# Performance work log

Measured on AMD Instinct MI355X. Metric: run time of the kernel, lower is better.

Reference implementation:

```python
import jax, jax.numpy as jnp
import numpy as np

B, N, DIM = 2, 2048, 2048
H, KVH, HD = 16, 4, 128
N_REP = H // KVH
SCALE = np.float32(HD ** -0.5)


def setup_inputs() -> dict:
    key = jax.random.key(0)
    ks = jax.random.split(key, 5)
    x = jax.random.normal(ks[0], (B, N, DIM), dtype=jnp.float32)
    mask = jnp.tril(jnp.ones((N, N), dtype=jnp.int32))[None, None]  # [1,1,N,N] causal
    Wq = jax.random.normal(ks[1], (DIM, H * HD), dtype=jnp.float32) * (DIM ** -0.5)
    Wk = jax.random.normal(ks[2], (DIM, KVH * HD), dtype=jnp.float32) * (DIM ** -0.5)
    Wv = jax.random.normal(ks[3], (DIM, KVH * HD), dtype=jnp.float32) * (DIM ** -0.5)
    Wo = jax.random.normal(ks[4], (H * HD, DIM), dtype=jnp.float32) * ((H * HD) ** -0.5)
    return {"x": x, "mask": mask, "Wq": Wq, "Wk": Wk, "Wv": Wv, "Wo": Wo}


def reference(x, mask, Wq, Wk, Wv, Wo):
    Bx, Nx, _ = x.shape
    # projections -> [B, heads, N, head_dim]
    q = (x @ Wq).reshape(Bx, Nx, H, HD).transpose(0, 2, 1, 3)
    k = (x @ Wk).reshape(Bx, Nx, KVH, HD).transpose(0, 2, 1, 3)
    v = (x @ Wv).reshape(Bx, Nx, KVH, HD).transpose(0, 2, 1, 3)
    # repeat_interleave KV heads to match query heads (GQA)
    k = jnp.repeat(k, N_REP, axis=1)
    v = jnp.repeat(v, N_REP, axis=1)
    attn = jnp.einsum('bhqd,bhkd->bhqk', q, k) * SCALE
    attn = jnp.where(mask == 0, jnp.float32(-jnp.inf), attn)
    attn = jax.nn.softmax(attn, axis=-1)
    out = jnp.einsum('bhqk,bhkd->bhqd', attn, v)
    out = out.transpose(0, 2, 1, 3).reshape(Bx, Nx, H * HD)
    return out @ Wo
```

## Files before the change

### kernel.cpp

```cpp
#include <hip/hip_runtime.h>
#include <hip/hip_bf16.h>
#include <math.h>

typedef __bf16 bf16;
typedef bf16 bf16x8 __attribute__((ext_vector_type(8)));
typedef bf16 bf16x4v __attribute__((ext_vector_type(4)));
typedef float f32x4 __attribute__((ext_vector_type(4)));

#define GLD16(g, l) __builtin_amdgcn_global_load_lds(                          \
    (__attribute__((address_space(1))) void*)(g),                              \
    (__attribute__((address_space(3))) void*)(l), 16, 0, 0)

#define MFMA16(a, b, c) __builtin_amdgcn_mfma_f32_16x16x32_bf16((a), (b), (c), 0, 0, 0)

__device__ __forceinline__ f32x4 shfl_xor4(f32x4 a, int m) {
  f32x4 r;
  #pragma unroll
  for (int i = 0; i < 4; i++) r[i] = __shfl_xor(a[i], m);
  return r;
}

__global__ void cast_f32_bf16(const float* __restrict__ in, bf16* __restrict__ out, int n4) {
  int i = blockIdx.x * blockDim.x + threadIdx.x;
  if (i < n4) {
    float4 v = ((const float4*)in)[i];
    bf16x4v o;
    o.x = (bf16)v.x; o.y = (bf16)v.y; o.z = (bf16)v.z; o.w = (bf16)v.w;
    ((bf16x4v*)out)[i] = o;
  }
}

__global__ void transpose_cast(const float* __restrict__ in, bf16* __restrict__ out,
                               int colsIn, int outStride, int outRowOff) {
  __shared__ float t[32][33];
  int c0 = blockIdx.x * 32, r0 = blockIdx.y * 32;
  int tx = threadIdx.x, ty = threadIdx.y;
  #pragma unroll
  for (int i = 0; i < 32; i += 8)
    t[ty + i][tx] = in[(size_t)(r0 + ty + i) * colsIn + (c0 + tx)];
  __syncthreads();
  #pragma unroll
  for (int i = 0; i < 32; i += 8)
    out[(size_t)(outRowOff + c0 + ty + i) * outStride + (r0 + tx)] = (bf16)t[tx][ty + i];
}

template <typename OutT>
__global__ __launch_bounds__(256, 2) void gemm_bt(const bf16* __restrict__ A,
                                                  const bf16* __restrict__ Bt,
                                                  OutT* __restrict__ C,
                                                  int M, int N, int K) {
  __shared__ __attribute__((aligned(16))) bf16 As[128 * 32];
  __shared__ __attribute__((aligned(16))) bf16 Bs[128 * 32];
  const int tid = threadIdx.x;
  const int lane = tid & 63;
  const int wave = tid >> 6;
  const int wm = wave >> 1, wn = wave & 1;
  const int l15 = lane & 15, quad = lane >> 4;
  const int rowBase = blockIdx.y * 128;
  const int colBase = blockIdx.x * 128;

  f32x4 acc[4][4] = {};

  const int cb0 = wave * 64;
  const int c0 = cb0 + lane;
  const int c1 = c0 + 256;
  const bf16* a0 = A + (size_t)(rowBase + (c0 >> 2)) * K + (c0 & 3) * 8;
  const bf16* a1 = A + (size_t)(rowBase + (c1 >> 2)) * K + (c1 & 3) * 8;
  const bf16* b0 = Bt + (size_t)(colBase + (c0 >> 2)) * K + (c0 & 3) * 8;
  const bf16* b1 = Bt + (size_t)(colBase + (c1 >> 2)) * K + (c1 & 3) * 8;
  bf16* lA0 = &As[cb0 * 8];
  bf16* lA1 = &As[(cb0 + 256) * 8];
  bf16* lB0 = &Bs[cb0 * 8];
  bf16* lB1 = &Bs[(cb0 + 256) * 8];

  for (int k0 = 0; k0 < K; k0 += 32) {
    GLD16(a0 + k0, lA0);
    GLD16(a1 + k0, lA1);
    GLD16(b0 + k0, lB0);
    GLD16(b1 + k0, lB1);
    __syncthreads();
    bf16x8 af[4], bfr[4];
    #pragma unroll
    for (int i = 0; i < 4; i++)
      af[i] = *(const bf16x8*)&As[(wm * 64 + i * 16 + l15) * 32 + quad * 8];
    #pragma unroll
    for (int i = 0; i < 4; i++)
      bfr[i] = *(const bf16x8*)&Bs[(wn * 64 + i * 16 + l15) * 32 + quad * 8];
    #pragma unroll
    for (int i = 0; i < 4; i++)
      #pragma unroll
      for (int j = 0; j < 4; j++)
        acc[i][j] = MFMA16(af[i], bfr[j], acc[i][j]);
    __syncthreads();
  }

  #pragma unroll
  for (int i = 0; i < 4; i++) {
    int row = rowBase + wm * 64 + i * 16 + quad * 4;
    #pragma unroll
    for (int j = 0; j < 4; j++) {
      int col = colBase + wn * 64 + j * 16 + l15;
      #pragma unroll
      for (int r = 0; r < 4; r++)
        C[(size_t)(row + r) * N + col] = (OutT)acc[i][j][r];
    }
  }
}

#define SCALE_F 0.08838834764831845f
#define L2E 1.4426950408889634f
#define MASKV (-1e30f)

__global__ __launch_bounds__(256, 2) void gqa_attn(const bf16* __restrict__ QKV,
                                                   bf16* __restrict__ Obf) {
  __shared__ __attribute__((aligned(16))) bf16 Kl[64 * 152];
  __shared__ __attribute__((aligned(16))) bf16 Vt[128 * 72];
  __shared__ __attribute__((aligned(16))) bf16 Pl[4][32 * 72];

  const int tid = threadIdx.x;
  const int lane = tid & 63;
  const int wave = tid >> 6;
  const int l15 = lane & 15, quad = lane >> 4;

  int bi = blockIdx.x;
  int bh = bi & 31;
  int jj = (bi & 255) >> 5;
  int qt = (bi < 256) ? (8 + jj) : (7 - jj);
  int b = bh >> 4, h = bh & 15, kvh = h >> 2;
  int q0 = qt * 128;

  const size_t rs = 3072;
  const bf16* Qb = QKV + (size_t)b * 2048 * rs + h * 128;
  const bf16* Kb = QKV + (size_t)b * 2048 * rs + 2048 + kvh * 128;
  const bf16* Vb = QKV + (size_t)b * 2048 * rs + 2560 + kvh * 128;

  bf16x8 qf[2][4];
  #pragma unroll
  for (int mt = 0; mt < 2; mt++) {
    int row = q0 + wave * 32 + mt * 16 + l15;
    #pragma unroll
    for (int ks = 0; ks < 4; ks++)
      qf[mt][ks] = *(const bf16x8*)&Qb[(size_t)row * rs + ks * 32 + quad * 8];
  }

  f32x4 oacc[2][8] = {};
  f32x4 mrow[2], lrow[2];
  #pragma unroll
  for (int mt = 0; mt < 2; mt++)
    #pragma unroll
    for (int r = 0; r < 4; r++) { mrow[mt][r] = MASKV; lrow[mt][r] = 0.f; }

  const int nkt = 2 * qt + 2;
  for (int kt = 0; kt < nkt; kt++) {
    const int k0 = kt * 64;
    __syncthreads();
    #pragma unroll
    for (int it = 0; it < 4; it++) {
      int c = it * 256 + tid;
      int key = c >> 4, hc = c & 15;
      bf16x8 v = *(const bf16x8*)&Kb[(size_t)(k0 + key) * rs + hc * 8];
      *(bf16x8*)&Kl[key * 152 + hc * 8] = v;
    }
    #pragma unroll
    for (int it = 0; it < 4; it++) {
      int c = it * 256 + tid;
      int key = c & 63, hc = c >> 6;
      bf16x8 v = *(const bf16x8*)&Vb[(size_t)(k0 + key) * rs + hc * 8];
      #pragma unroll
      for (int j2 = 0; j2 < 8; j2++) Vt[(hc * 8 + j2) * 72 + key] = v[j2];
    }
    __syncthreads();

    if (k0 > q0 + wave * 32 + 31) continue;

    f32x4 s[2][4] = {};
    #pragma unroll
    for (int nt = 0; nt < 4; nt++) {
      #pragma unroll
      for (int ks = 0; ks < 4; ks++) {
        bf16x8 kf = *(const bf16x8*)&Kl[(nt * 16 + l15) * 152 + ks * 32 + quad * 8];
        s[0][nt] = MFMA16(qf[0][ks], kf, s[0][nt]);
        s[1][nt] = MFMA16(qf[1][ks], kf, s[1][nt]);
      }
    }
    bool diag = (kt >= nkt - 2);
    #pragma unroll
    for (int mt = 0; mt < 2; mt++)
      #pragma unroll
      for (int nt = 0; nt < 4; nt++)
        #pragma unroll
        for (int r = 0; r < 4; r++) {
          float v = s[mt][nt][r] * SCALE_F;
          if (diag) {
            int col = k0 + nt * 16 + l15;
            int row = q0 + wave * 32 + mt * 16 + quad * 4 + r;
            if (col > row) v = MASKV;
          }
          s[mt][nt][r] = v;
        }
    #pragma unroll
    for (int mt = 0; mt < 2; mt++) {
      f32x4 mx = s[mt][0];
      #pragma unroll
      for (int nt = 1; nt < 4; nt++)
        #pragma unroll
        for (int r = 0; r < 4; r++) mx[r] = fmaxf(mx[r], s[mt][nt][r]);
      #pragma unroll
      for (int d = 1; d < 16; d <<= 1) {
        f32x4 o = shfl_xor4(mx, d);
        #pragma unroll
        for (int r = 0; r < 4; r++) mx[r] = fmaxf(mx[r], o[r]);
      }
      f32x4 mnew, alpha;
      #pragma unroll
      for (int r = 0; r < 4; r++) {
        mnew[r] = fmaxf(mrow[mt][r], mx[r]);
        alpha[r] = exp2f((mrow[mt][r] - mnew[r]) * L2E);
      }
      f32x4 rsum = {0.f, 0.f, 0.f, 0.f};
      #pragma unroll
      for (int nt = 0; nt < 4; nt++)
        #pragma unroll
        for (int r = 0; r < 4; r++) {
          float p = exp2f((s[mt][nt][r] - mnew[r]) * L2E);
          s[mt][nt][r] = p;
          rsum[r] += p;
        }
      #pragma unroll
      for (int d = 1; d < 16; d <<= 1) rsum += shfl_xor4(rsum, d);
      #pragma unroll
      for (int r = 0; r < 4; r++) {
        lrow[mt][r] = lrow[mt][r] * alpha[r] + rsum[r];
        mrow[mt][r] = mnew[r];
      }
      #pragma unroll
      for (int no = 0; no < 8; no++)
        #pragma unroll
        for (int r = 0; r < 4; r++) oacc[mt][no][r] *= alpha[r];
      #pragma unroll
      for (int nt = 0; nt < 4; nt++)
        #pragma unroll
        for (int r = 0; r < 4; r++)
          Pl[wave][(mt * 16 + quad * 4 + r) * 72 + nt * 16 + l15] = (bf16)s[mt][nt][r];
    }
    #pragma unroll
    for (int ks2 = 0; ks2 < 2; ks2++) {
      bf16x8 pf0 = *(const bf16x8*)&Pl[wave][(l15) * 72 + ks2 * 32 + quad * 8];
      bf16x8 pf1 = *(const bf16x8*)&Pl[wave][(16 + l15) * 72 + ks2 * 32 + quad * 8];
      #pragma unroll
      for (int no = 0; no < 8; no++) {
        bf16x8 vf = *(const bf16x8*)&Vt[(no * 16 + l15) * 72 + ks2 * 32 + quad * 8];
        oacc[0][no] = MFMA16(pf0, vf, oacc[0][no]);
        oacc[1][no] = MFMA16(pf1, vf, oacc[1][no]);
      }
    }
  }

  #pragma unroll
  for (int mt = 0; mt < 2; mt++) {
    f32x4 linv;
    #pragma unroll
    for (int r = 0; r < 4; r++) linv[r] = 1.0f / lrow[mt][r];
    int row = q0 + wave * 32 + mt * 16 + quad * 4;
    #pragma unroll
    for (int no = 0; no < 8; no++) {
      int col = h * 128 + no * 16 + l15;
      #pragma unroll
      for (int r = 0; r < 4; r++)
        Obf[(size_t)(b * 2048 + row + r) * 2048 + col] = (bf16)(oacc[mt][no][r] * linv[r]);
    }
  }
}

extern "C" void kernel_launch(void* const* d_in, const int* in_sizes, int n_in,
                              void* d_out, int out_size, void* d_ws, size_t ws_size,
                              hipStream_t stream) {
  const float* x  = (const float*)d_in[0];
  const float* Wq = (const float*)d_in[2];
  const float* Wk = (const float*)d_in[3];
  const float* Wv = (const float*)d_in[4];
  const float* Wo = (const float*)d_in[5];
  float* out = (float*)d_out;

  bf16* Xb    = (bf16*)d_ws;
  bf16* Wqkvt = Xb + 8388608;
  bf16* Wot   = Wqkvt + 6291456;
  bf16* QKV   = Wot + 4194304;
  bf16* Obf   = QKV + 12582912;

  cast_f32_bf16<<<8192, 256, 0, stream>>>(x, Xb, 2097152);
  dim3 tb(32, 8);
  transpose_cast<<<dim3(64, 64), tb, 0, stream>>>(Wq, Wqkvt, 2048, 2048, 0);
  transpose_cast<<<dim3(16, 64), tb, 0, stream>>>(Wk, Wqkvt, 512, 2048, 2048);
  transpose_cast<<<dim3(16, 64), tb, 0, stream>>>(Wv, Wqkvt, 512, 2048, 2560);
  transpose_cast<<<dim3(64, 64), tb, 0, stream>>>(Wo, Wot, 2048, 2048, 0);

  gemm_bt<bf16><<<dim3(24, 32), 256, 0, stream>>>(Xb, Wqkvt, QKV, 4096, 3072, 2048);
  gqa_attn<<<512, 256, 0, stream>>>(QKV, Obf);
  gemm_bt<float><<<dim3(16, 32), 256, 0, stream>>>(Obf, Wot, out, 4096, 2048, 2048);
}
```

Measured before the change: 368.8 us.

## Pre-transpose V, load K/V tiles via direct-to-LDS loads with XOR swizzle

Adds a separate kernel that transposes V into a head-major [d, n] buffer. The attention kernel can then fill its K and V tiles with asynchronous global_load_lds 16-byte copies into XOR-swizzled LDS, replacing the register round trip and scalar scatter transpose of V. The softmax scale and log2(e) are folded into Wq during the weight cast, and a native exp2 builtin is used, which removes per-element multiplies. The cost is an extra kernel launch plus one read and write of V, and bf16 rounding of the pre-scaled Wq differs slightly from the original.

```diff
diff --git a/kernel.cpp b/kernel.cpp
--- a/kernel.cpp
+++ b/kernel.cpp
@@ -12,6 +12,12 @@
     (__attribute__((address_space(3))) void*)(l), 16, 0, 0)
 
 #define MFMA16(a, b, c) __builtin_amdgcn_mfma_f32_16x16x32_bf16((a), (b), (c), 0, 0, 0)
+
+#if __has_builtin(__builtin_amdgcn_exp2f)
+#define EXP2F(x) __builtin_amdgcn_exp2f(x)
+#else
+#define EXP2F(x) exp2f(x)
+#endif
 
 __device__ __forceinline__ f32x4 shfl_xor4(f32x4 a, int m) {
   f32x4 r;
@@ -31,7 +37,7 @@
 }
 
 __global__ void transpose_cast(const float* __restrict__ in, bf16* __restrict__ out,
-                               int colsIn, int outStride, int outRowOff) {
+                               int colsIn, int outStride, int outRowOff, float scale) {
   __shared__ float t[32][33];
   int c0 = blockIdx.x * 32, r0 = blockIdx.y * 32;
   int tx = threadIdx.x, ty = threadIdx.y;
@@ -41,7 +47,24 @@
   __syncthreads();
   #pragma unroll
   for (int i = 0; i < 32; i += 8)
-    out[(size_t)(outRowOff + c0 + ty + i) * outStride + (r0 + tx)] = (bf16)t[tx][ty + i];
+    out[(size_t)(outRowOff + c0 + ty + i) * outStride + (r0 + tx)] = (bf16)(t[tx][ty + i] * scale);
+}
+
+__global__ void transpose_v(const bf16* __restrict__ QKV, bf16* __restrict__ Vg) {
+  __shared__ bf16 t[32][34];
+  int n0 = blockIdx.x * 32, d0 = blockIdx.y * 32;
+  int bk = blockIdx.z;
+  int b = bk >> 2, kvh = bk & 3;
+  const bf16* src = QKV + (size_t)b * 2048 * 3072 + 2560 + kvh * 128;
+  bf16* dst = Vg + (size_t)bk * 128 * 2048;
+  int tx = threadIdx.x, ty = threadIdx.y;
+  #pragma unroll
+  for (int i = 0; i < 32; i += 8)
+    t[ty + i][tx] = src[(size_t)(n0 + ty + i) * 3072 + (d0 + tx)];
+  __syncthreads();
+  #pragma unroll
+  for (int i = 0; i < 32; i += 8)
+    dst[(size_t)(d0 + ty + i) * 2048 + (n0 + tx)] = t[tx][ty + i];
 }
 
 template <typename OutT>
@@ -107,15 +130,14 @@
   }
 }
 
-#define SCALE_F 0.08838834764831845f
-#define L2E 1.4426950408889634f
 #define MASKV (-1e30f)
 
 __global__ __launch_bounds__(256, 2) void gqa_attn(const bf16* __restrict__ QKV,
+                                                   const bf16* __restrict__ Vg,
                                                    bf16* __restrict__ Obf) {
-  __shared__ __attribute__((aligned(16))) bf16 Kl[64 * 152];
-  __shared__ __attribute__((aligned(16))) bf16 Vt[128 * 72];
-  __shared__ __attribute__((aligned(16))) bf16 Pl[4][32 * 72];
+  __shared__ __attribute__((aligned(16))) bf16 Kl[64 * 128];
+  __shared__ __attribute__((aligned(16))) bf16 Vt[128 * 64];
+  __shared__ __attribute__((aligned(16))) bf16 Pl[4][32 * 68];
 
   const int tid = threadIdx.x;
   const int lane = tid & 63;
@@ -130,9 +152,9 @@
   int q0 = qt * 128;
 
   const size_t rs = 3072;
-  const bf16* Qb = QKV + (size_t)b * 2048 * rs + h * 128;
-  const bf16* Kb = QKV + (size_t)b * 2048 * rs + 2048 + kvh * 128;
-  const bf16* Vb = QKV + (size_t)b * 2048 * rs + 2560 + kvh * 128;
+  const bf16* Qb  = QKV + (size_t)b * 2048 * rs + h * 128;
+  const bf16* Kb  = QKV + (size_t)b * 2048 * rs + 2048 + kvh * 128;
+  const bf16* Vgb = Vg + (size_t)(b * 4 + kvh) * 128 * 2048;
 
   bf16x8 qf[2][4];
   #pragma unroll
@@ -143,6 +165,20 @@
       qf[mt][ks] = *(const bf16x8*)&Qb[(size_t)row * rs + ks * 32 + quad * 8];
   }
 
+  const bf16* kp[4]; const bf16* vp[4];
+  bf16* kl[4]; bf16* vl[4];
+  #pragma unroll
+  for (int t = 0; t < 4; t++) {
+    int keyl = wave * 16 + t * 4 + (lane >> 4);
+    int ck = (lane & 15) ^ (4 * (t & 1) + (lane >> 4));
+    kp[t] = Kb + (size_t)keyl * rs + ck * 8;
+    kl[t] = &Kl[(wave * 16 + t * 4) * 128];
+    int dl = wave * 32 + t * 8 + (lane >> 3);
+    int cv = (lane & 7) ^ (lane >> 3);
+    vp[t] = Vgb + (size_t)dl * 2048 + cv * 8;
+    vl[t] = &Vt[(wave * 32 + t * 8) * 64];
+  }
+
   f32x4 oacc[2][8] = {};
   f32x4 mrow[2], lrow[2];
   #pragma unroll
@@ -151,53 +187,42 @@
     for (int r = 0; r < 4; r++) { mrow[mt][r] = MASKV; lrow[mt][r] = 0.f; }
 
   const int nkt = 2 * qt + 2;
+  const int myrow_hi = q0 + wave * 32 + 31;
   for (int kt = 0; kt < nkt; kt++) {
     const int k0 = kt * 64;
     __syncthreads();
     #pragma unroll
-    for (int it = 0; it < 4; it++) {
-      int c = it * 256 + tid;
-      int key = c >> 4, hc = c & 15;
-      bf16x8 v = *(const bf16x8*)&Kb[(size_t)(k0 + key) * rs + hc * 8];
-      *(bf16x8*)&Kl[key * 152 + hc * 8] = v;
-    }
-    #pragma unroll
-    for (int it = 0; it < 4; it++) {
-      int c = it * 256 + tid;
-      int key = c & 63, hc = c >> 6;
-      bf16x8 v = *(const bf16x8*)&Vb[(size_t)(k0 + key) * rs + hc * 8];
-      #pragma unroll
-      for (int j2 = 0; j2 < 8; j2++) Vt[(hc * 8 + j2) * 72 + key] = v[j2];
-    }
+    for (int t = 0; t < 4; t++) { GLD16(kp[t], kl[t]); kp[t] += 64 * rs; }
+    #pragma unroll
+    for (int t = 0; t < 4; t++) { GLD16(vp[t], vl[t]); vp[t] += 64; }
     __syncthreads();
 
-    if (k0 > q0 + wave * 32 + 31) continue;
+    if (k0 > myrow_hi) continue;
 
     f32x4 s[2][4] = {};
     #pragma unroll
-    for (int nt = 0; nt < 4; nt++) {
-      #pragma unroll
-      for (int ks = 0; ks < 4; ks++) {
-        bf16x8 kf = *(const bf16x8*)&Kl[(nt * 16 + l15) * 152 + ks * 32 + quad * 8];
+    for (int ks = 0; ks < 4; ks++) {
+      #pragma unroll
+      for (int nt = 0; nt < 4; nt++) {
+        bf16x8 kf = *(const bf16x8*)&Kl[(nt * 16 + l15) * 128 +
+                                        (((ks * 4 + quad) ^ (l15 & 7)) * 8)];
         s[0][nt] = MFMA16(qf[0][ks], kf, s[0][nt]);
         s[1][nt] = MFMA16(qf[1][ks], kf, s[1][nt]);
       }
     }
-    bool diag = (kt >= nkt - 2);
-    #pragma unroll
-    for (int mt = 0; mt < 2; mt++)
-      #pragma unroll
-      for (int nt = 0; nt < 4; nt++)
-        #pragma unroll
-        for (int r = 0; r < 4; r++) {
-          float v = s[mt][nt][r] * SCALE_F;
-          if (diag) {
-            int col = k0 + nt * 16 + l15;
-            int row = q0 + wave * 32 + mt * 16 + quad * 4 + r;
-            if (col > row) v = MASKV;
-          }
-          s[mt][nt][r] = v;
+    if (kt >= nkt - 2) {
+      #pragma unroll
+      for (int mt = 0; mt < 2; mt++) {
+        int rowb = q0 + wave * 32 + mt * 16 + quad * 4;
+        #pragma unroll
+        for (int nt = 0; nt < 4; nt++) {
+          int col = k0 + nt * 16 + l15;
+          #pragma unroll
+          for (int r = 0; r < 4; r++)
+            if (col > rowb + r) s[mt][nt][r] = MASKV;
         }
+      }
+    }
     #pragma unroll
     for (int mt = 0; mt < 2; mt++) {
       f32x4 mx = s[mt][0];
@@ -215,14 +240,14 @@
       #pragma unroll
       for (int r = 0; r < 4; r++) {
         mnew[r] = fmaxf(mrow[mt][r], mx[r]);
-        alpha[r] = exp2f((mrow[mt][r] - mnew[r]) * L2E);
+        alpha[r] = EXP2F(mrow[mt][r] - mnew[r]);
       }
       f32x4 rsum = {0.f, 0.f, 0.f, 0.f};
       #pragma unroll
       for (int nt = 0; nt < 4; nt++)
         #pragma unroll
         for (int r = 0; r < 4; r++) {
-          float p = exp2f((s[mt][nt][r] - mnew[r]) * L2E);
+          float p = EXP2F(s[mt][nt][r] - mnew[r]);
           s[mt][nt][r] = p;
           rsum[r] += p;
         }
@@ -241,15 +266,16 @@
       for (int nt = 0; nt < 4; nt++)
         #pragma unroll
         for (int r = 0; r < 4; r++)
-          Pl[wave][(mt * 16 + quad * 4 + r) * 72 + nt * 16 + l15] = (bf16)s[mt][nt][r];
+          Pl[wave][(mt * 16 + quad * 4 + r) * 68 + nt * 16 + l15] = (bf16)s[mt][nt][r];
     }
     #pragma unroll
     for (int ks2 = 0; ks2 < 2; ks2++) {
-      bf16x8 pf0 = *(const bf16x8*)&Pl[wave][(l15) * 72 + ks2 * 32 + quad * 8];
-      bf16x8 pf1 = *(const bf16x8*)&Pl[wave][(16 + l15) * 72 + ks2 * 32 + quad * 8];
+      bf16x8 pf0 = *(const bf16x8*)&Pl[wave][l15 * 68 + ks2 * 32 + quad * 8];
+      bf16x8 pf1 = *(const bf16x8*)&Pl[wave][(16 + l15) * 68 + ks2 * 32 + quad * 8];
       #pragma unroll
       for (int no = 0; no < 8; no++) {
-        bf16x8 vf = *(const bf16x8*)&Vt[(no * 16 + l15) * 72 + ks2 * 32 + quad * 8];
+        bf16x8 vf = *(const bf16x8*)&Vt[(no * 16 + l15) * 64 +
+                                        (((ks2 * 4 + quad) ^ (l15 & 7)) * 8)];
         oacc[0][no] = MFMA16(pf0, vf, oacc[0][no]);
         oacc[1][no] = MFMA16(pf1, vf, oacc[1][no]);
       }
@@ -287,15 +313,19 @@
   bf16* Wot   = Wqkvt + 6291456;
   bf16* QKV   = Wot + 4194304;
   bf16* Obf   = QKV + 12582912;
+  bf16* Vg    = Obf + 8388608;
+
+  const float qscale = (float)(0.08838834764831845 * 1.4426950408889634);
 
   cast_f32_bf16<<<8192, 256, 0, stream>>>(x, Xb, 2097152);
   dim3 tb(32, 8);
-  transpose_cast<<<dim3(64, 64), tb, 0, stream>>>(Wq, Wqkvt, 2048, 2048, 0);
-  transpose_cast<<<dim3(16, 64), tb, 0, stream>>>(Wk, Wqkvt, 512, 2048, 2048);
-  transpose_cast<<<dim3(16, 64), tb, 0, stream>>>(Wv, Wqkvt, 512, 2048, 2560);
-  transpose_cast<<<dim3(64, 64), tb, 0, stream>>>(Wo, Wot, 2048, 2048, 0);
+  transpose_cast<<<dim3(64, 64), tb, 0, stream>>>(Wq, Wqkvt, 2048, 2048, 0, qscale);
+  transpose_cast<<<dim3(16, 64), tb, 0, stream>>>(Wk, Wqkvt, 512, 2048, 2048, 1.0f);
+  transpose_cast<<<dim3(16, 64), tb, 0, stream>>>(Wv, Wqkvt, 512, 2048, 2560, 1.0f);
+  transpose_cast<<<dim3(64, 64), tb, 0, stream>>>(Wo, Wot, 2048, 2048, 0, 1.0f);
 
   gemm_bt<bf16><<<dim3(24, 32), 256, 0, stream>>>(Xb, Wqkvt, QKV, 4096, 3072, 2048);
-  gqa_attn<<<512, 256, 0, stream>>>(QKV, Obf);
+  transpose_v<<<dim3(64, 4, 8), tb, 0, stream>>>(QKV, Vg);
+  gqa_attn<<<512, 256, 0, stream>>>(QKV, Vg, Obf);
   gemm_bt<float><<<dim3(16, 32), 256, 0, stream>>>(Obf, Wot, out, 4096, 2048, 2048);
 }
```

Measured after the change: 339.0 us. 1.09x faster.
